# Optimization experiments

Measured on AMD Instinct MI355X. Metric: run time of the kernel, lower is better.

The kernel has to match this reference:

```python
import jax, jax.numpy as jnp
import numpy as np

N_NODES = 50000
N_EDGES = 800000
D_IN = 100
HID = 128
N_LAYERS = 3
N_GRAPHS = 64


def setup_inputs() -> dict:
    key = jax.random.key(0)
    ks = jax.random.split(key, 10)
    x = jax.random.normal(ks[0], (N_NODES, D_IN), dtype=jnp.float32)
    edge_index = jax.random.randint(ks[1], (2, N_EDGES), 0, N_NODES, dtype=jnp.int64)
    batch = jnp.sort(jax.random.randint(ks[2], (N_NODES,), 0, N_GRAPHS, dtype=jnp.int64))
    s = 1.0 / np.sqrt(D_IN)
    W_enc = jax.random.uniform(ks[3], (D_IN, HID), jnp.float32, -s, s)
    b_enc = jax.random.uniform(ks[4], (HID,), jnp.float32, -s, s)
    sh = 1.0 / np.sqrt(HID)
    gcn_W = jax.random.uniform(ks[5], (N_LAYERS, HID, HID), jnp.float32, -sh, sh)
    gcn_b = jax.random.uniform(ks[6], (N_LAYERS, HID), jnp.float32, -sh, sh)
    W_reg = jax.random.uniform(ks[7], (HID, 1), jnp.float32, -sh, sh)
    b_reg = jax.random.uniform(ks[8], (1,), jnp.float32, -sh, sh)
    return {"x": x, "edge_index": edge_index, "batch": batch,
            "W_enc": W_enc, "b_enc": b_enc, "gcn_W": gcn_W, "gcn_b": gcn_b,
            "W_reg": W_reg, "b_reg": b_reg}


def reference(x, edge_index, batch, W_enc, b_enc, gcn_W, gcn_b, W_reg, b_reg):
    N = x.shape[0]
    # node encoder
    h = x @ W_enc + b_enc  # [N, HID]
    # GCN normalization with self-loops (edge_weight = 1, PyG gcn_norm)
    loop = jnp.arange(N, dtype=edge_index.dtype)
    src = jnp.concatenate([edge_index[0], loop])  # [E+N]
    dst = jnp.concatenate([edge_index[1], loop])
    deg = jax.ops.segment_sum(jnp.ones_like(src, dtype=h.dtype), dst, num_segments=N)
    dinv = jnp.where(deg > 0, jax.lax.rsqrt(deg), 0.0)
    norm = dinv[src] * dinv[dst]  # [E+N]
    for i in range(N_LAYERS):
        m = (h @ gcn_W[i])[src] * norm[:, None]           # gather + scale messages
        h = jax.ops.segment_sum(m, dst, num_segments=N)   # scatter-add aggregate
        h = jax.nn.relu(h + gcn_b[i])
    # global mean pool over graphs
    sums = jax.ops.segment_sum(h, batch, num_segments=N_GRAPHS)
    cnt = jax.ops.segment_sum(jnp.ones((N,), dtype=h.dtype), batch, num_segments=N_GRAPHS)
    pooled = sums / jnp.maximum(cnt, 1.0)[:, None]        # [N_GRAPHS, HID]
    return pooled @ W_reg + b_reg                         # [N_GRAPHS, 1]
```

## Files before the change

### kernel.cpp

```cpp
#include <hip/hip_runtime.h>
#include <hip/hip_fp16.h>

#define N_NODES 50000
#define N_EDGES 800000
#define D_INN 100
#define HID 128
#define N_GRAPHS 64
#define NBLK ((N_NODES + 255) / 256)
#define POOL_ROWS 128
#define POOL_BLOCKS ((N_NODES + POOL_ROWS - 1) / POOL_ROWS)

#define NBUCK 8
#define NODES_PER_BUCK (N_NODES / NBUCK)
#define SCAT_BLOCKS 2048

typedef _Float16 f16x8 __attribute__((ext_vector_type(8)));
typedef float f32x4 __attribute__((ext_vector_type(4)));

__global__ void k_init(int* __restrict__ deg, float* __restrict__ sums) {
    int i = blockIdx.x * 256 + threadIdx.x;
    if (i < N_NODES) deg[i] = 1;
    if (i < N_GRAPHS * HID) sums[i] = 0.f;
}

__global__ __launch_bounds__(256) void k_deg(const int* __restrict__ dst,
                                             int* __restrict__ deg) {
    int b = blockIdx.x & (NBUCK - 1);
    int lo = b * NODES_PER_BUCK, hi = lo + NODES_PER_BUCK;
    int sub = blockIdx.x >> 3, nsub = gridDim.x >> 3;
    for (int e = sub * 256 + threadIdx.x; e < N_EDGES; e += nsub * 256) {
        int d = dst[e];
        if (d >= lo && d < hi) atomicAdd(&deg[d], 1);
    }
}

__global__ __launch_bounds__(256) void k_scan1(const int* __restrict__ deg,
                                               int* __restrict__ incl,
                                               int* __restrict__ bsums) {
    __shared__ int sm[256];
    int i = blockIdx.x * 256 + threadIdx.x;
    int v = (i < N_NODES) ? deg[i] : 0;
    sm[threadIdx.x] = v;
    __syncthreads();
    for (int off = 1; off < 256; off <<= 1) {
        int t = (threadIdx.x >= off) ? sm[threadIdx.x - off] : 0;
        __syncthreads();
        sm[threadIdx.x] += t;
        __syncthreads();
    }
    if (i < N_NODES) incl[i] = sm[threadIdx.x];
    if (threadIdx.x == 255) bsums[blockIdx.x] = sm[255];
}

__global__ __launch_bounds__(256) void k_scan2(const int* __restrict__ bsums,
                                               int* __restrict__ boff) {
    __shared__ int sm[256];
    int v = (threadIdx.x < NBLK) ? bsums[threadIdx.x] : 0;
    sm[threadIdx.x] = v;
    __syncthreads();
    for (int off = 1; off < 256; off <<= 1) {
        int t = (threadIdx.x >= off) ? sm[threadIdx.x - off] : 0;
        __syncthreads();
        sm[threadIdx.x] += t;
        __syncthreads();
    }
    boff[threadIdx.x] = sm[threadIdx.x] - v;
}

__global__ void k_scan3(const int* __restrict__ incl, const int* __restrict__ boff,
                        const int* __restrict__ deg, int* __restrict__ offsets,
                        int* __restrict__ cursor, int* __restrict__ csr_src,
                        float* __restrict__ dinv) {
    int i = blockIdx.x * 256 + threadIdx.x;
    if (i < N_NODES) {
        int off1 = incl[i] + boff[blockIdx.x];
        offsets[i + 1] = off1;
        int dg = deg[i];
        int p0 = off1 - dg;
        csr_src[p0] = i;
        cursor[i] = p0 + 1;
        dinv[i] = rsqrtf((float)dg);
    }
    if (i == 0) offsets[0] = 0;
}

__global__ __launch_bounds__(256) void k_fill(const int* __restrict__ src,
                                              const int* __restrict__ dst,
                                              int* __restrict__ cursor,
                                              int* __restrict__ csr_src) {
    int b = blockIdx.x & (NBUCK - 1);
    int lo = b * NODES_PER_BUCK, hi = lo + NODES_PER_BUCK;
    int sub = blockIdx.x >> 3, nsub = gridDim.x >> 3;
    for (int e = sub * 256 + threadIdx.x; e < N_EDGES; e += nsub * 256) {
        int d = dst[e];
        if (d >= lo && d < hi) {
            int s = src[e];
            int p = atomicAdd(&cursor[d], 1);
            csr_src[p] = s;
        }
    }
}

__global__ void k_wts(const float* __restrict__ W, const float* __restrict__ We,
                      __half* __restrict__ Wt, __half* __restrict__ Wte) {
    int i = blockIdx.x * 256 + threadIdx.x;
    if (i < 3 * HID * HID) {
        int l = i >> 14, rem = i & 16383;
        int c = rem >> 7, k = rem & 127;
        Wt[(l << 14) + c * HID + k] = __float2half(W[(l << 14) + k * HID + c]);
    } else if (i < 4 * HID * HID) {
        int j = i - 3 * HID * HID;
        int c = j >> 7, k = j & 127;
        float v = (k < D_INN) ? We[k * HID + c] : 0.f;
        Wte[c * HID + k] = __float2half(v);
    }
}

__global__ void k_xh(const float* __restrict__ x, __half2* __restrict__ xh) {
    int i = blockIdx.x * 256 + threadIdx.x;
    if (i < N_NODES * 64) {
        int r = i >> 6, c = (i & 63) * 2;
        float v0 = (c     < D_INN) ? x[r * D_INN + c]     : 0.f;
        float v1 = (c + 1 < D_INN) ? x[r * D_INN + c + 1] : 0.f;
        xh[i] = __floats2half2_rn(v0, v1);
    }
}

template <bool BIAS, bool DINV>
__global__ __launch_bounds__(256) void k_gemm_mfma(const _Float16* __restrict__ A,
                                                   const _Float16* __restrict__ Wt,
                                                   const float* __restrict__ bias,
                                                   const float* __restrict__ dinv,
                                                   _Float16* __restrict__ out) {
    const int lane = threadIdx.x & 63;
    const int wave = threadIdx.x >> 6;
    const int l15  = lane & 15;
    const int lhi  = lane >> 4;
    f16x8 bf0[4], bf1[4];
#pragma unroll
    for (int ks = 0; ks < 4; ++ks) {
        int col0 = wave * 32 + l15;
        int col1 = wave * 32 + 16 + l15;
        bf0[ks] = *(const f16x8*)(Wt + col0 * HID + ks * 32 + lhi * 8);
        bf1[ks] = *(const f16x8*)(Wt + col1 * HID + ks * 32 + lhi * 8);
    }
    float b0 = 0.f, b1 = 0.f;
    if (BIAS) {
        b0 = bias[wave * 32 + l15];
        b1 = bias[wave * 32 + 16 + l15];
    }
    for (int chunk = blockIdx.x; chunk < N_NODES / 16; chunk += gridDim.x) {
        int row0 = chunk * 16;
        const _Float16* Ar = A + (row0 + l15) * HID + lhi * 8;
        f16x8 af0 = *(const f16x8*)(Ar);
        f16x8 af1 = *(const f16x8*)(Ar + 32);
        f16x8 af2 = *(const f16x8*)(Ar + 64);
        f16x8 af3 = *(const f16x8*)(Ar + 96);
        f32x4 acc0 = {0.f, 0.f, 0.f, 0.f};
        f32x4 acc1 = {0.f, 0.f, 0.f, 0.f};
        acc0 = __builtin_amdgcn_mfma_f32_16x16x32_f16(af0, bf0[0], acc0, 0, 0, 0);
        acc1 = __builtin_amdgcn_mfma_f32_16x16x32_f16(af0, bf1[0], acc1, 0, 0, 0);
        acc0 = __builtin_amdgcn_mfma_f32_16x16x32_f16(af1, bf0[1], acc0, 0, 0, 0);
        acc1 = __builtin_amdgcn_mfma_f32_16x16x32_f16(af1, bf1[1], acc1, 0, 0, 0);
        acc0 = __builtin_amdgcn_mfma_f32_16x16x32_f16(af2, bf0[2], acc0, 0, 0, 0);
        acc1 = __builtin_amdgcn_mfma_f32_16x16x32_f16(af2, bf1[2], acc1, 0, 0, 0);
        acc0 = __builtin_amdgcn_mfma_f32_16x16x32_f16(af3, bf0[3], acc0, 0, 0, 0);
        acc1 = __builtin_amdgcn_mfma_f32_16x16x32_f16(af3, bf1[3], acc1, 0, 0, 0);
#pragma unroll
        for (int r = 0; r < 4; ++r) {
            int row = row0 + lhi * 4 + r;
            float v0 = acc0[r] + b0;
            float v1 = acc1[r] + b1;
            if (DINV) {
                float dr = dinv[row];
                v0 *= dr; v1 *= dr;
            }
            out[row * HID + wave * 32 + l15]      = (_Float16)v0;
            out[row * HID + wave * 32 + 16 + l15] = (_Float16)v1;
        }
    }
}

__global__ __launch_bounds__(256) void k_agg(const __half* __restrict__ B,
                                             const int* __restrict__ offsets,
                                             const int* __restrict__ csr_src,
                                             const float* __restrict__ dinv,
                                             const float* __restrict__ bias,
                                             __half* __restrict__ A) {
    int node = (blockIdx.x * 256 + threadIdx.x) >> 6;
    int lane = threadIdx.x & 63;
    if (node >= N_NODES) return;
    int beg = offsets[node], end = offsets[node + 1];
    float ax0 = 0.f, ay0 = 0.f, ax1 = 0.f, ay1 = 0.f;
    const __half2* B2 = (const __half2*)B;
    int j = beg;
    while (j < end) {
        int take = end - j; if (take > 64) take = 64;
        int s_l = (lane < take) ? csr_src[j + lane] : 0;
        int t = 0;
        for (; t + 4 <= take; t += 4) {
            int s0 = __shfl(s_l, t + 0), s1 = __shfl(s_l, t + 1);
            int s2 = __shfl(s_l, t + 2), s3 = __shfl(s_l, t + 3);
            float2 f0 = __half22float2(B2[s0 * 64 + lane]);
            float2 f1 = __half22float2(B2[s1 * 64 + lane]);
            float2 f2 = __half22float2(B2[s2 * 64 + lane]);
            float2 f3 = __half22float2(B2[s3 * 64 + lane]);
            ax0 += f0.x; ay0 += f0.y;
            ax1 += f1.x; ay1 += f1.y;
            ax0 += f2.x; ay0 += f2.y;
            ax1 += f3.x; ay1 += f3.y;
        }
        for (; t < take; ++t) {
            int s = __shfl(s_l, t);
            float2 f = __half22float2(B2[s * 64 + lane]);
            ax0 += f.x; ay0 += f.y;
        }
        j += take;
    }
    float dn = dinv[node];
    float2 b = ((const float2*)bias)[lane];
    float rx = fmaxf(fmaf(dn, ax0 + ax1, b.x), 0.f);
    float ry = fmaxf(fmaf(dn, ay0 + ay1, b.y), 0.f);
    ((__half2*)A)[node * 64 + lane] = __floats2half2_rn(rx, ry);
}

__global__ __launch_bounds__(64) void k_pool_part(const __half* __restrict__ A,
                                                  const int* __restrict__ batch,
                                                  float* __restrict__ sums) {
    int base = blockIdx.x * POOL_ROWS;
    if (base >= N_NODES) return;
    int c = threadIdx.x;
    int end = base + POOL_ROWS;
    if (end > N_NODES) end = N_NODES;
    const __half2* A2 = (const __half2*)A;
    float ax = 0.f, ay = 0.f;
    int g = batch[base];
    for (int n = base; n < end; ++n) {
        int bg = batch[n];
        if (bg != g) {
            atomicAdd(&sums[g * HID + 2 * c], ax);
            atomicAdd(&sums[g * HID + 2 * c + 1], ay);
            ax = 0.f; ay = 0.f;
            g = bg;
        }
        float2 f = __half22float2(A2[n * 64 + c]);
        ax += f.x; ay += f.y;
    }
    atomicAdd(&sums[g * HID + 2 * c], ax);
    atomicAdd(&sums[g * HID + 2 * c + 1], ay);
}

__global__ __launch_bounds__(128) void k_head(const float* __restrict__ sums,
                                              const int* __restrict__ batch,
                                              const float* __restrict__ W_reg,
                                              const float* __restrict__ b_reg,
                                              float* __restrict__ out) {
    int g = blockIdx.x;
    int lo = 0, hi = N_NODES;
    while (lo < hi) { int mid = (lo + hi) >> 1; if (batch[mid] < g) lo = mid + 1; else hi = mid; }
    int start = lo;
    hi = N_NODES;
    while (lo < hi) { int mid = (lo + hi) >> 1; if (batch[mid] < g + 1) lo = mid + 1; else hi = mid; }
    int end = lo;
    float cnt = (float)((end - start) > 0 ? (end - start) : 1);
    float v = (sums[g * HID + threadIdx.x] / cnt) * W_reg[threadIdx.x];
    for (int off = 32; off > 0; off >>= 1) v += __shfl_down(v, off);
    __shared__ float sm[2];
    if ((threadIdx.x & 63) == 0) sm[threadIdx.x >> 6] = v;
    __syncthreads();
    if (threadIdx.x == 0) out[g] = sm[0] + sm[1] + b_reg[0];
}

extern "C" void kernel_launch(void* const* d_in, const int* in_sizes, int n_in,
                              void* d_out, int out_size, void* d_ws, size_t ws_size,
                              hipStream_t stream) {
    const float* x      = (const float*)d_in[0];
    const int*   e_src  = (const int*)d_in[1];
    const int*   e_dst  = e_src + N_EDGES;
    const int*   batch  = (const int*)d_in[2];
    const float* W_enc  = (const float*)d_in[3];
    const float* b_enc  = (const float*)d_in[4];
    const float* gcn_W  = (const float*)d_in[5];
    const float* gcn_b  = (const float*)d_in[6];
    const float* W_reg  = (const float*)d_in[7];
    const float* b_reg  = (const float*)d_in[8];
    float* out = (float*)d_out;

    char* p = (char*)d_ws;
    auto carve = [&](size_t bytes) { char* q = p; p += (bytes + 255) & ~(size_t)255; return q; };
    __half* hA      = (__half*)carve(sizeof(__half) * N_NODES * HID);
    __half* msg     = (__half*)carve(sizeof(__half) * N_NODES * HID);
    __half* xh      = (__half*)carve(sizeof(__half) * N_NODES * HID);
    __half* Wt      = (__half*)carve(sizeof(__half) * 3 * HID * HID);
    __half* Wte     = (__half*)carve(sizeof(__half) * HID * HID);
    int*    csr_src = (int*)   carve(sizeof(int)    * (N_EDGES + N_NODES));
    int*    deg     = (int*)   carve(sizeof(int)    * N_NODES);
    int*    cursor  = (int*)   carve(sizeof(int)    * N_NODES);
    int*    offsets = (int*)   carve(sizeof(int)    * (N_NODES + 1));
    int*    incl    = (int*)   carve(sizeof(int)    * N_NODES);
    int*    bsums   = (int*)   carve(sizeof(int)    * 256);
    int*    boff    = (int*)   carve(sizeof(int)    * 256);
    float*  dinv    = (float*) carve(sizeof(float)  * N_NODES);
    float*  sums    = (float*) carve(sizeof(float)  * N_GRAPHS * HID);

    k_init<<<NBLK, 256, 0, stream>>>(deg, sums);
    k_deg<<<SCAT_BLOCKS, 256, 0, stream>>>(e_dst, deg);
    k_scan1<<<NBLK, 256, 0, stream>>>(deg, incl, bsums);
    k_scan2<<<1, 256, 0, stream>>>(bsums, boff);
    k_scan3<<<NBLK, 256, 0, stream>>>(incl, boff, deg, offsets, cursor, csr_src, dinv);
    k_fill<<<SCAT_BLOCKS, 256, 0, stream>>>(e_src, e_dst, cursor, csr_src);

    k_wts<<<(4 * HID * HID + 255) / 256, 256, 0, stream>>>(gcn_W, W_enc, Wt, Wte);
    k_xh<<<(N_NODES * 64 + 255) / 256, 256, 0, stream>>>(x, (__half2*)xh);

    k_gemm_mfma<true, false><<<640, 256, 0, stream>>>(
        (const _Float16*)xh, (const _Float16*)Wte, b_enc, nullptr, (_Float16*)hA);
    for (int l = 0; l < 3; ++l) {
        k_gemm_mfma<false, true><<<640, 256, 0, stream>>>(
            (const _Float16*)hA, (const _Float16*)(Wt + l * HID * HID), nullptr, dinv,
            (_Float16*)msg);
        k_agg<<<(N_NODES * 64 + 255) / 256, 256, 0, stream>>>(
            msg, offsets, csr_src, dinv, gcn_b + l * HID, hA);
    }
    k_pool_part<<<POOL_BLOCKS, 64, 0, stream>>>(hA, batch, sums);
    k_head<<<N_GRAPHS, 128, 0, stream>>>(sums, batch, W_reg, b_reg, out);
}
```

Before: 376.1 us.

## Store node features in column-blocked layout so aggregation gathers fit cache per block

Node feature matrices now use a column-blocked layout: 8 blocks of 16 fp16 columns, each block stored contiguously across all nodes. This touches the input conversion, the MFMA GEMM loads and stores, and pooling. Aggregation now launches one wave per node per column block, with 8 edges handled in parallel by lane groups and a shuffle reduction at the end. The goal is a smaller random-gather working set per column block (about 1.6MB), so gathers hit in cache more often. In exchange, the CSR index reads are repeated 8 times, there are more blocks, and the per-edge gather granularity drops to 32 bytes per edge.

```diff
diff --git a/kernel.cpp b/kernel.cpp
--- a/kernel.cpp
+++ b/kernel.cpp
@@ -13,6 +13,10 @@
 #define NBUCK 8
 #define NODES_PER_BUCK (N_NODES / NBUCK)
 #define SCAT_BLOCKS 2048
+
+#define CB_STRIDE  (N_NODES * 16)
+#define CB_STRIDE2 (N_NODES * 8)
+#define AGG_BLOCKS (NBUCK * (N_NODES / 4))
 
 typedef _Float16 f16x8 __attribute__((ext_vector_type(8)));
 typedef float f32x4 __attribute__((ext_vector_type(4)));
@@ -119,10 +123,11 @@
 __global__ void k_xh(const float* __restrict__ x, __half2* __restrict__ xh) {
     int i = blockIdx.x * 256 + threadIdx.x;
     if (i < N_NODES * 64) {
-        int r = i >> 6, c = (i & 63) * 2;
+        int r = i >> 6, c2 = i & 63;
+        int c = c2 * 2;
         float v0 = (c     < D_INN) ? x[r * D_INN + c]     : 0.f;
         float v1 = (c + 1 < D_INN) ? x[r * D_INN + c + 1] : 0.f;
-        xh[i] = __floats2half2_rn(v0, v1);
+        xh[(c2 >> 3) * CB_STRIDE2 + r * 8 + (c2 & 7)] = __floats2half2_rn(v0, v1);
     }
 }
 
@@ -149,13 +154,15 @@
         b0 = bias[wave * 32 + l15];
         b1 = bias[wave * 32 + 16 + l15];
     }
+    const int bsel = lhi >> 1;
+    const int boffs = (lhi & 1) * 8;
     for (int chunk = blockIdx.x; chunk < N_NODES / 16; chunk += gridDim.x) {
         int row0 = chunk * 16;
-        const _Float16* Ar = A + (row0 + l15) * HID + lhi * 8;
-        f16x8 af0 = *(const f16x8*)(Ar);
-        f16x8 af1 = *(const f16x8*)(Ar + 32);
-        f16x8 af2 = *(const f16x8*)(Ar + 64);
-        f16x8 af3 = *(const f16x8*)(Ar + 96);
+        const _Float16* Ar = A + (row0 + l15) * 16 + boffs;
+        f16x8 af0 = *(const f16x8*)(Ar + (0 + bsel) * CB_STRIDE);
+        f16x8 af1 = *(const f16x8*)(Ar + (2 + bsel) * CB_STRIDE);
+        f16x8 af2 = *(const f16x8*)(Ar + (4 + bsel) * CB_STRIDE);
+        f16x8 af3 = *(const f16x8*)(Ar + (6 + bsel) * CB_STRIDE);
         f32x4 acc0 = {0.f, 0.f, 0.f, 0.f};
         f32x4 acc1 = {0.f, 0.f, 0.f, 0.f};
         acc0 = __builtin_amdgcn_mfma_f32_16x16x32_f16(af0, bf0[0], acc0, 0, 0, 0);
@@ -175,79 +182,78 @@
                 float dr = dinv[row];
                 v0 *= dr; v1 *= dr;
             }
-            out[row * HID + wave * 32 + l15]      = (_Float16)v0;
-            out[row * HID + wave * 32 + 16 + l15] = (_Float16)v1;
+            out[(wave * 2    ) * CB_STRIDE + row * 16 + l15] = (_Float16)v0;
+            out[(wave * 2 + 1) * CB_STRIDE + row * 16 + l15] = (_Float16)v1;
         }
     }
 }
 
-__global__ __launch_bounds__(256) void k_agg(const __half* __restrict__ B,
+__global__ __launch_bounds__(256) void k_agg(const __half2* __restrict__ Bcb,
                                              const int* __restrict__ offsets,
                                              const int* __restrict__ csr_src,
                                              const float* __restrict__ dinv,
                                              const float* __restrict__ bias,
-                                             __half* __restrict__ A) {
-    int node = (blockIdx.x * 256 + threadIdx.x) >> 6;
+                                             __half2* __restrict__ Acb) {
+    int b = blockIdx.x & (NBUCK - 1);
+    int node = (blockIdx.x >> 3) * 4 + (threadIdx.x >> 6);
     int lane = threadIdx.x & 63;
-    if (node >= N_NODES) return;
+    int col = lane & 7;
+    int esl = lane >> 3;
+    const __half2* Bb = Bcb + b * CB_STRIDE2;
     int beg = offsets[node], end = offsets[node + 1];
-    float ax0 = 0.f, ay0 = 0.f, ax1 = 0.f, ay1 = 0.f;
-    const __half2* B2 = (const __half2*)B;
+    float ax = 0.f, ay = 0.f;
     int j = beg;
     while (j < end) {
         int take = end - j; if (take > 64) take = 64;
-        int s_l = (lane < take) ? csr_src[j + lane] : 0;
-        int t = 0;
-        for (; t + 4 <= take; t += 4) {
-            int s0 = __shfl(s_l, t + 0), s1 = __shfl(s_l, t + 1);
-            int s2 = __shfl(s_l, t + 2), s3 = __shfl(s_l, t + 3);
-            float2 f0 = __half22float2(B2[s0 * 64 + lane]);
-            float2 f1 = __half22float2(B2[s1 * 64 + lane]);
-            float2 f2 = __half22float2(B2[s2 * 64 + lane]);
-            float2 f3 = __half22float2(B2[s3 * 64 + lane]);
-            ax0 += f0.x; ay0 += f0.y;
-            ax1 += f1.x; ay1 += f1.y;
-            ax0 += f2.x; ay0 += f2.y;
-            ax1 += f3.x; ay1 += f3.y;
-        }
-        for (; t < take; ++t) {
-            int s = __shfl(s_l, t);
-            float2 f = __half22float2(B2[s * 64 + lane]);
-            ax0 += f.x; ay0 += f.y;
+        int s8 = (lane < take) ? (csr_src[j + lane] << 3) : -8;
+        int ng = (take + 7) >> 3;
+        for (int g = 0; g < ng; ++g) {
+            int si = __shfl(s8, (g << 3) + esl);
+            if (si >= 0) {
+                float2 f = __half22float2(Bb[si + col]);
+                ax += f.x; ay += f.y;
+            }
         }
         j += take;
     }
-    float dn = dinv[node];
-    float2 b = ((const float2*)bias)[lane];
-    float rx = fmaxf(fmaf(dn, ax0 + ax1, b.x), 0.f);
-    float ry = fmaxf(fmaf(dn, ay0 + ay1, b.y), 0.f);
-    ((__half2*)A)[node * 64 + lane] = __floats2half2_rn(rx, ry);
-}
-
-__global__ __launch_bounds__(64) void k_pool_part(const __half* __restrict__ A,
+    ax += __shfl_xor(ax, 8);  ay += __shfl_xor(ay, 8);
+    ax += __shfl_xor(ax, 16); ay += __shfl_xor(ay, 16);
+    ax += __shfl_xor(ax, 32); ay += __shfl_xor(ay, 32);
+    if (esl == 0) {
+        float dn = dinv[node];
+        int cg = (b << 4) + (col << 1);
+        float rx = fmaxf(fmaf(dn, ax, bias[cg]), 0.f);
+        float ry = fmaxf(fmaf(dn, ay, bias[cg + 1]), 0.f);
+        Acb[b * CB_STRIDE2 + node * 8 + col] = __floats2half2_rn(rx, ry);
+    }
+}
+
+__global__ __launch_bounds__(64) void k_pool_part(const __half2* __restrict__ A2,
                                                   const int* __restrict__ batch,
                                                   float* __restrict__ sums) {
     int base = blockIdx.x * POOL_ROWS;
     if (base >= N_NODES) return;
-    int c = threadIdx.x;
+    int c2 = threadIdx.x;
+    int b = c2 >> 3, off = c2 & 7;
+    int cg = (b << 4) + (off << 1);
+    const __half2* Ab = A2 + b * CB_STRIDE2;
     int end = base + POOL_ROWS;
     if (end > N_NODES) end = N_NODES;
-    const __half2* A2 = (const __half2*)A;
     float ax = 0.f, ay = 0.f;
     int g = batch[base];
     for (int n = base; n < end; ++n) {
         int bg = batch[n];
         if (bg != g) {
-            atomicAdd(&sums[g * HID + 2 * c], ax);
-            atomicAdd(&sums[g * HID + 2 * c + 1], ay);
+            atomicAdd(&sums[g * HID + cg], ax);
+            atomicAdd(&sums[g * HID + cg + 1], ay);
             ax = 0.f; ay = 0.f;
             g = bg;
         }
-        float2 f = __half22float2(A2[n * 64 + c]);
+        float2 f = __half22float2(Ab[n * 8 + off]);
         ax += f.x; ay += f.y;
     }
-    atomicAdd(&sums[g * HID + 2 * c], ax);
-    atomicAdd(&sums[g * HID + 2 * c + 1], ay);
+    atomicAdd(&sums[g * HID + cg], ax);
+    atomicAdd(&sums[g * HID + cg + 1], ay);
 }
 
 __global__ __launch_bounds__(128) void k_head(const float* __restrict__ sums,
@@ -319,9 +325,10 @@
         k_gemm_mfma<false, true><<<640, 256, 0, stream>>>(
             (const _Float16*)hA, (const _Float16*)(Wt + l * HID * HID), nullptr, dinv,
             (_Float16*)msg);
-        k_agg<<<(N_NODES * 64 + 255) / 256, 256, 0, stream>>>(
-            msg, offsets, csr_src, dinv, gcn_b + l * HID, hA);
-    }
-    k_pool_part<<<POOL_BLOCKS, 64, 0, stream>>>(hA, batch, sums);
+        k_agg<<<AGG_BLOCKS, 256, 0, stream>>>(
+            (const __half2*)msg, offsets, csr_src, dinv, gcn_b + l * HID,
+            (__half2*)hA);
+    }
+    k_pool_part<<<POOL_BLOCKS, 64, 0, stream>>>((const __half2*)hA, batch, sums);
     k_head<<<N_GRAPHS, 128, 0, stream>>>(sums, batch, W_reg, b_reg, out);
 }
```

Result: slower. 574.7 us (+52.8%).
